# Performance work log

Measured on AMD Instinct MI355X. Metric: run time of the kernel, lower is better.

The kernel has to match this reference:

```python
import jax, jax.numpy as jnp
import numpy as np
from jax import lax


def squash(s):
    # scale = |s|^2/(1+|s|^2); out = scale * s/|s| (eps-stabilized as in source)
    norm = jnp.sum(s * s, axis=-1, keepdims=True)
    return (norm / (1.0 + norm)) * (s / jnp.sqrt(norm + 1e-8))


def setup_inputs() -> dict:
    key = jax.random.key(0)
    k = jax.random.split(key, 4)
    B, H, C = 32, 64, 10
    x = jax.random.normal(k[0], (B, 3, H, H), jnp.float32)
    conv1_w = jax.random.normal(k[1], (256, 3, 9, 9), jnp.float32) * 0.06
    conv1_b = jnp.zeros((256,), jnp.float32)
    conv2_w = jax.random.normal(k[2], (256, 256, 9, 9), jnp.float32) * 0.02  # 256 = 8 caps * 32 routes
    conv2_b = jnp.zeros((256,), jnp.float32)
    route_w = jax.random.normal(k[3], (32, C, 8, 16), jnp.float32)  # [routes, classes, in_dim, out_dim]
    return {"x": x, "conv1_w": conv1_w, "conv1_b": conv1_b,
            "conv2_w": conv2_w, "conv2_b": conv2_b, "route_w": route_w}


def reference(x, conv1_w, conv1_b, conv2_w, conv2_b, route_w):
    dn = ("NCHW", "OIHW", "NCHW")
    # PrimaryCapsules: conv 3->256 k9 s1 + relu
    h = lax.conv_general_dilated(x, conv1_w, (1, 1), "VALID", dimension_numbers=dn)
    h = jax.nn.relu(h + conv1_b[None, :, None, None])
    # CapsuleLayer conv: 256 -> 8*32 k9 s2
    h = lax.conv_general_dilated(h, conv2_w, (2, 2), "VALID", dimension_numbers=dn)
    h = h + conv2_b[None, :, None, None]
    B, _, hh, ww = h.shape
    R, D = 32, 8  # num_routes, capsule dim
    # [B, R*D, h, w] -> [B, R, P, D], squash per capsule vector
    caps = h.reshape(B, R, D, hh, ww).transpose(0, 1, 3, 4, 2).reshape(B, R, hh * ww, D)
    caps = squash(caps)
    # DigitCapsules: per-route linear maps 8->16, shared over spatial positions
    u_hat = jnp.einsum("brpi,rcio->brpco", caps, route_w)  # [B, R, P, C, 16]
    C, O = u_hat.shape[3], u_hat.shape[4]
    u_hat = u_hat.reshape(B, R * hh * ww, C, O)  # [B, N, C, 16]
    b_log = jnp.zeros(u_hat.shape[:-1], u_hat.dtype)  # [B, N, C]
    num_routing = 3
    v = None
    for i in range(num_routing):
        c = jax.nn.softmax(b_log, axis=2)            # over classes (dim=2 in source)
        s = jnp.einsum("bnc,bnco->bco", c, u_hat)    # weighted sum over input caps
        v = squash(s)                                 # [B, C, 16]
        if i < num_routing - 1:
            b_log = b_log + jnp.einsum("bnco,bco->bnc", u_hat, v)  # agreement
    return v
```

## Files before the change

kernel.cpp:

```cpp
#include <hip/hip_runtime.h>
#include <hip/hip_bf16.h>
#include <stdint.h>

typedef __attribute__((ext_vector_type(8))) short short8;
typedef __attribute__((ext_vector_type(4))) float f32x4;
typedef unsigned int u32x4a __attribute__((vector_size(16)));
typedef unsigned int u32x4u __attribute__((vector_size(16), aligned(4)));

__device__ inline unsigned short f2bf(float f) {
    union { float f; uint32_t u; } v; v.f = f;
    uint32_t u = v.u;
    uint32_t r = (u + 0x7FFFu + ((u >> 16) & 1u)) >> 16;
    return (unsigned short)r;
}

__device__ inline void gl_lds16(const unsigned short* g, unsigned short* l) {
    __builtin_amdgcn_global_load_lds(
        (const uint32_t __attribute__((address_space(1)))*)(const void*)g,
        (uint32_t __attribute__((address_space(3)))*)(void*)l, 16, 0, 0);
}

__global__ void cvt_w1(const float* __restrict__ w, unsigned short* __restrict__ A1) {
    int idx = blockIdx.x * 256 + threadIdx.x;
    int row = idx >> 8, k = idx & 255;
    float v = (k < 243) ? w[row * 243 + k] : 0.f;
    A1[idx] = f2bf(v);
}

__global__ void cvt_w2(const float* __restrict__ w, unsigned short* __restrict__ A2t) {
    int idx = blockIdx.x * 256 + threadIdx.x;
    int j = idx & 7;
    int off16 = (idx >> 3) & 1023;
    int tile = idx >> 13;
    int tm = tile / 324, chunk = tile - tm * 324;
    int row = off16 >> 3, sw = off16 & 7;
    int koct = sw ^ (row & 7);
    int kk = chunk * 64 + koct * 8 + j;
    int oc = tm * 128 + row;
    int ic, ky, kx;
    if (kk < 18432) { ic = kk / 72; int rem = kk - ic * 72; ky = rem >> 3; kx = rem & 7; }
    else { int j2 = kk - 18432; ic = j2 / 9; ky = j2 - ic * 9; kx = 8; }
    A2t[idx] = f2bf(w[((oc * 256 + ic) * 9 + ky) * 9 + kx]);
}

__global__ __launch_bounds__(256) void conv1_gemm(
    const unsigned short* __restrict__ A,
    const float* __restrict__ x,
    const float* __restrict__ bias,
    unsigned short* __restrict__ h1)
{
    __shared__ __align__(16) unsigned short As[128 * 40];
    __shared__ __align__(16) unsigned short Bs[128 * 40];
    const int tid = threadIdx.x;
    const int m0 = blockIdx.y * 128;
    const int n0 = blockIdx.x * 128;
    const int lane = tid & 63;
    const int wave = tid >> 6;
    const int wy = wave & 1, wx = wave >> 1;
    const int l16 = lane & 15, q = lane >> 4;

    const int kp = tid & 15;
    const int gn = tid >> 4;
    int baseN[8];
#pragma unroll
    for (int j = 0; j < 8; ++j) {
        int n = n0 + gn * 8 + j;
        int b = n / 3136, p = n % 3136;
        int oy = p / 56, ox = p % 56;
        baseN[j] = b * 12288 + oy * 64 + ox;
    }

    f32x4 acc[4][4];
#pragma unroll
    for (int im = 0; im < 4; ++im)
#pragma unroll
        for (int in = 0; in < 4; ++in)
            acc[im][in] = (f32x4){0.f, 0.f, 0.f, 0.f};

    for (int k0 = 0; k0 < 256; k0 += 32) {
        __syncthreads();
#pragma unroll
        for (int s = 0; s < 2; ++s) {
            int slot = tid + s * 256;
            int row = slot >> 2, seg = slot & 3;
            u32x4a v = *(const u32x4a*)(A + (m0 + row) * 256 + k0 + seg * 8);
            *(u32x4a*)(&As[row * 40 + seg * 8]) = v;
        }
        int ka = k0 + 2 * kp, kb = ka + 1;
        int offa = 0, offb = 0;
        bool va = ka < 243, vb = kb < 243;
        if (va) { int c = ka / 81, t = ka % 81, ky = t / 9, kx = t % 9; offa = c * 4096 + ky * 64 + kx; }
        if (vb) { int c = kb / 81, t = kb % 81, ky = t / 9, kx = t % 9; offb = c * 4096 + ky * 64 + kx; }
#pragma unroll
        for (int j = 0; j < 8; ++j) {
            unsigned int ba = va ? (unsigned int)f2bf(x[baseN[j] + offa]) : 0u;
            unsigned int bb = vb ? (unsigned int)f2bf(x[baseN[j] + offb]) : 0u;
            *(unsigned int*)(&Bs[(gn * 8 + j) * 40 + 2 * kp]) = ba | (bb << 16);
        }
        __syncthreads();

        short8 af[4], bf[4];
#pragma unroll
        for (int im = 0; im < 4; ++im)
            af[im] = *(const short8*)(&As[(wy * 64 + im * 16 + l16) * 40 + q * 8]);
#pragma unroll
        for (int in = 0; in < 4; ++in)
            bf[in] = *(const short8*)(&Bs[(wx * 64 + in * 16 + l16) * 40 + q * 8]);
#pragma unroll
        for (int im = 0; im < 4; ++im)
#pragma unroll
            for (int in = 0; in < 4; ++in)
                acc[im][in] = __builtin_amdgcn_mfma_f32_16x16x32_bf16(af[im], bf[in], acc[im][in], 0, 0, 0);
    }

#pragma unroll
    for (int in = 0; in < 4; ++in) {
        int n = n0 + wx * 64 + in * 16 + l16;
        int b = n / 3136, p = n % 3136;
        int oy = p / 56, ox = p % 56;
#pragma unroll
        for (int im = 0; im < 4; ++im) {
#pragma unroll
            for (int r = 0; r < 4; ++r) {
                int oc = m0 + wy * 64 + im * 16 + q * 4 + r;
                float v = acc[im][in][r] + bias[oc];
                v = v > 0.f ? v : 0.f;
                h1[((b * 256 + oc) * 56 + oy) * 56 + ox] = f2bf(v);
            }
        }
    }
}

#define C2ROW 72
__global__ __launch_bounds__(256) void conv2_gemm(
    const unsigned short* __restrict__ A2t,
    const unsigned short* __restrict__ h1,
    float* __restrict__ c2)
{
    __shared__ __align__(16) unsigned short As[2][8192];
    __shared__ __align__(16) unsigned short Bs[128 * C2ROW];
    const int tid = threadIdx.x;
    const int n0 = blockIdx.x * 128;
    const int z = blockIdx.z;
    const int lane = tid & 63;
    const int wave = tid >> 6;
    const int wy = wave & 1, wx = wave >> 1;
    const int l16 = lane & 15, q = lane >> 4;

    const int oct = tid >> 5;
    int bsrc[4], bdst[4];
#pragma unroll
    for (int i = 0; i < 4; ++i) {
        int n = (tid & 31) + 32 * i;
        int ng = n0 + n;
        int b = ng / 576, p = ng % 576;
        int oy = p / 24, ox = p % 24;
        bsrc[i] = b * 802816 + (2 * oy) * 56 + 2 * ox;
        bdst[i] = n * C2ROW + oct * 8;
    }
    const int tn = tid & 127, thalf = tid >> 7;
    int tbase;
    {
        int ng = n0 + tn;
        int b = ng / 576, p = ng % 576;
        int oy = p / 24, ox = p % 24;
        tbase = b * 802816 + (2 * oy) * 56 + 2 * ox + 8;
    }

    f32x4 acc[4][4];
#pragma unroll
    for (int im = 0; im < 4; ++im)
#pragma unroll
        for (int in = 0; in < 4; ++in)
            acc[im][in] = (f32x4){0.f, 0.f, 0.f, 0.f};

    const size_t tilebase = (size_t)blockIdx.y * 324 * 8192;
    uint32_t bR[16];

    auto issueA = [&](int c, int buf) {
        const unsigned short* at = A2t + tilebase + (size_t)c * 8192;
        int s0 = wave * 4;
#pragma unroll
        for (int i = 0; i < 4; ++i) {
            int sl = (s0 + i) * 64 + lane;
            gl_lds16(at + sl * 8, &As[buf][sl * 8]);
        }
    };
    auto loadB = [&](int c) {
        if (c < 288) {
            int octk = c * 8 + oct;
            int ic = octk / 9, ky = octk - ic * 9;
            int off = ic * 3136 + ky * 56;
#pragma unroll
            for (int i = 0; i < 4; ++i) {
                u32x4u v = *(const u32x4u*)(h1 + bsrc[i] + off);
                bR[4 * i + 0] = v[0]; bR[4 * i + 1] = v[1];
                bR[4 * i + 2] = v[2]; bR[4 * i + 3] = v[3];
            }
        } else {
            int base = c * 64 + thalf * 32 - 18432;
#pragma unroll
            for (int p = 0; p < 16; ++p) {
                int j2 = base + 2 * p;
                int icA = j2 / 9, kyA = j2 - icA * 9;
                int icB = (j2 + 1) / 9, kyB = (j2 + 1) - icB * 9;
                uint32_t ba = h1[tbase + icA * 3136 + kyA * 56];
                uint32_t bb = h1[tbase + icB * 3136 + kyB * 56];
                bR[p] = ba | (bb << 16);
            }
        }
    };
    auto writeB = [&](int c) {
        if (c < 288) {
#pragma unroll
            for (int i = 0; i < 4; ++i) {
                u32x4a v = {bR[4 * i], bR[4 * i + 1], bR[4 * i + 2], bR[4 * i + 3]};
                *(u32x4a*)(&Bs[bdst[i]]) = v;
            }
        } else {
#pragma unroll
            for (int p = 0; p < 16; ++p)
                *(uint32_t*)(&Bs[tn * C2ROW + thalf * 32 + 2 * p]) = bR[p];
        }
    };

    const int nch = (324 - z + 7) >> 3;
    int c = z;
    issueA(c, 0);
    loadB(c);
    for (int i = 0; i < nch; ++i) {
        const int cur = i & 1;
        const int ccur = c, cnext = c + 8;
        __asm__ volatile("s_waitcnt vmcnt(0)" ::: "memory");
        __syncthreads();
        writeB(ccur);
        __syncthreads();
        if (i + 1 < nch) { issueA(cnext, cur ^ 1); loadB(cnext); }
#pragma unroll
        for (int h = 0; h < 2; ++h) {
            short8 af[4], bf[4];
#pragma unroll
            for (int im = 0; im < 4; ++im) {
                int row = wy * 64 + im * 16 + l16;
                int koct = h * 4 + q;
                af[im] = *(const short8*)(&As[cur][(row * 8 + (koct ^ (row & 7))) * 8]);
            }
#pragma unroll
            for (int in = 0; in < 4; ++in)
                bf[in] = *(const short8*)(&Bs[(wx * 64 + in * 16 + l16) * C2ROW + h * 32 + q * 8]);
#pragma unroll
            for (int im = 0; im < 4; ++im)
#pragma unroll
                for (int in = 0; in < 4; ++in)
                    acc[im][in] = __builtin_amdgcn_mfma_f32_16x16x32_bf16(af[im], bf[in], acc[im][in], 0, 0, 0);
        }
        c = cnext;
    }

    const int m0 = blockIdx.y * 128;
#pragma unroll
    for (int in = 0; in < 4; ++in) {
        int nn = n0 + wx * 64 + in * 16 + l16;
        int bb = nn / 576, pp = nn % 576;
#pragma unroll
        for (int im = 0; im < 4; ++im) {
#pragma unroll
            for (int r = 0; r < 4; ++r) {
                int oc = m0 + wy * 64 + im * 16 + q * 4 + r;
                atomicAdd(&c2[(bb * 256 + oc) * 576 + pp], acc[im][in][r]);
            }
        }
    }
}

__global__ void squash_caps(const float* __restrict__ c2, const float* __restrict__ bias,
                            float* __restrict__ caps) {
    int idx = blockIdx.x * 256 + threadIdx.x;
    int b = idx / 18432;
    int rp = idx % 18432;
    int r = rp / 576, p = rp % 576;
    float s[8]; float n2 = 0.f;
#pragma unroll
    for (int d = 0; d < 8; ++d) {
        s[d] = c2[(b * 256 + r * 8 + d) * 576 + p] + bias[r * 8 + d];
        n2 += s[d] * s[d];
    }
    float sc = (n2 / (1.f + n2)) / sqrtf(n2 + 1e-8f);
#pragma unroll
    for (int d = 0; d < 8; ++d)
        caps[idx * 8 + d] = sc * s[d];
}

__global__ __launch_bounds__(64) void capsum0(const float* __restrict__ caps,
                                              float* __restrict__ G) {
    int r = blockIdx.x, b = blockIdx.y;
    const float* cp = caps + (size_t)(b * 32 + r) * 4608;
    int tid = threadIdx.x;
    f32x4 s0 = (f32x4){0.f, 0.f, 0.f, 0.f}, s1 = s0;
    for (int jv = 0; jv < 9; ++jv) {
        const f32x4* qp = (const f32x4*)(cp + (jv * 64 + tid) * 8);
        s0 += qp[0]; s1 += qp[1];
    }
#pragma unroll
    for (int off = 32; off > 0; off >>= 1) {
#pragma unroll
        for (int k = 0; k < 4; ++k) {
            s0[k] += __shfl_down(s0[k], off, 64);
            s1[k] += __shfl_down(s1[k], off, 64);
        }
    }
    if (tid == 0) {
        float g[8] = {s0[0], s0[1], s0[2], s0[3], s1[0], s1[1], s1[2], s1[3]};
        float* gp = G + (size_t)((b * 32 + r) * 10) * 8;
        for (int cc = 0; cc < 10; ++cc)
#pragma unroll
            for (int ii = 0; ii < 8; ++ii) gp[cc * 8 + ii] = g[ii] * 0.1f;
    }
}

__global__ __launch_bounds__(64) void route_accum(const float* __restrict__ caps,
                                                  const float* __restrict__ W,
                                                  const float* __restrict__ V,
                                                  float* __restrict__ G) {
    int r = blockIdx.x, b = blockIdx.y;
    __shared__ float wv[80];
    __shared__ float red[80][64];
    int tid = threadIdx.x;
    for (int v = tid; v < 80; v += 64) {
        int cc = v >> 3, ii = v & 7;
        float s = 0.f;
#pragma unroll
        for (int o = 0; o < 16; ++o)
            s += W[((r * 10 + cc) * 8 + ii) * 16 + o] * V[(b * 10 + cc) * 16 + o];
        wv[v] = s;
    }
    __syncthreads();
    float g[80];
#pragma unroll
    for (int v = 0; v < 80; ++v) g[v] = 0.f;
    const float* cp = caps + (size_t)(b * 32 + r) * 4608;
    for (int j = 0; j < 9; ++j) {
        int p = j * 64 + tid;
        const f32x4* qp = (const f32x4*)(cp + p * 8);
        f32x4 c0 = qp[0], c1 = qp[1];
        float c8[8];
#pragma unroll
        for (int i = 0; i < 4; ++i) { c8[i] = c0[i]; c8[4 + i] = c1[i]; }
        float a[10]; float m = -1e30f;
#pragma unroll
        for (int cc = 0; cc < 10; ++cc) {
            float t = 0.f;
#pragma unroll
            for (int i = 0; i < 8; ++i) t += c8[i] * wv[cc * 8 + i];
            a[cc] = t; m = fmaxf(m, t);
        }
        float sum = 0.f;
#pragma unroll
        for (int cc = 0; cc < 10; ++cc) { a[cc] = __expf(a[cc] - m); sum += a[cc]; }
        float inv = 1.f / sum;
#pragma unroll
        for (int cc = 0; cc < 10; ++cc) {
            float w = a[cc] * inv;
#pragma unroll
            for (int i = 0; i < 8; ++i) g[cc * 8 + i] += w * c8[i];
        }
    }
#pragma unroll
    for (int v = 0; v < 80; ++v) red[v][tid] = g[v];
    __syncthreads();
    for (int v = tid; v < 80; v += 64) {
        float s = 0.f;
        for (int t = 0; t < 64; ++t) s += red[v][t];
        G[(b * 32 + r) * 80 + v] = s;
    }
}

__global__ __launch_bounds__(160) void sv_kernel(const float* __restrict__ G,
                                                 const float* __restrict__ W,
                                                 float* __restrict__ V,
                                                 float* __restrict__ out, int last) {
    int b = blockIdx.x;
    int c = threadIdx.x / 16, o = threadIdx.x % 16;
    __shared__ float sL[10][16];
    float s = 0.f;
    for (int r = 0; r < 32; ++r) {
        const float* g = G + ((b * 32 + r) * 10 + c) * 8;
        const float* w = W + ((r * 10 + c) * 8) * 16 + o;
#pragma unroll
        for (int i = 0; i < 8; ++i) s += g[i] * w[i * 16];
    }
    sL[c][o] = s;
    __syncthreads();
    float n2 = 0.f;
#pragma unroll
    for (int oo = 0; oo < 16; ++oo) { float t = sL[c][oo]; n2 += t * t; }
    float sc = (n2 / (1.f + n2)) / sqrtf(n2 + 1e-8f);
    float v = sc * s;
    V[(b * 10 + c) * 16 + o] += v;
    if (last) out[(b * 10 + c) * 16 + o] = v;
}

extern "C" void kernel_launch(void* const* d_in, const int* in_sizes, int n_in,
                              void* d_out, int out_size, void* d_ws, size_t ws_size,
                              hipStream_t stream) {
    const float* x  = (const float*)d_in[0];
    const float* w1 = (const float*)d_in[1];
    const float* b1 = (const float*)d_in[2];
    const float* w2 = (const float*)d_in[3];
    const float* b2 = (const float*)d_in[4];
    const float* rw = (const float*)d_in[5];

    char* ws = (char*)d_ws;
    unsigned short* A1   = (unsigned short*)(ws);
    unsigned short* A2   = (unsigned short*)(ws + 262144);
    unsigned short* h1   = (unsigned short*)(ws + 10878976);
    float*          c2   = (float*)(ws + 62259200);
    float*          caps = (float*)(ws + 81133568);
    float*          V    = (float*)(ws + 100007936);
    float*          G    = (float*)(ws + 100028416);

    hipLaunchKernelGGL(cvt_w1, dim3(256), dim3(256), 0, stream, w1, A1);
    hipLaunchKernelGGL(cvt_w2, dim3(20736), dim3(256), 0, stream, w2, A2);
    hipMemsetAsync(c2, 0, 18874368, stream);
    hipLaunchKernelGGL(conv1_gemm, dim3(784, 2), dim3(256), 0, stream, A1, x, b1, h1);
    hipLaunchKernelGGL(conv2_gemm, dim3(144, 2, 8), dim3(256), 0, stream, A2, h1, c2);
    hipLaunchKernelGGL(squash_caps, dim3(2304), dim3(256), 0, stream, c2, b2, caps);
    hipMemsetAsync(V, 0, 5120 * sizeof(float), stream);
    hipLaunchKernelGGL(capsum0, dim3(32, 32), dim3(64), 0, stream, caps, G);
    hipLaunchKernelGGL(sv_kernel, dim3(32), dim3(160), 0, stream, G, rw, V, (float*)d_out, 0);
    for (int it = 1; it < 3; ++it) {
        hipLaunchKernelGGL(route_accum, dim3(32, 32), dim3(64), 0, stream, caps, rw, V, G);
        hipLaunchKernelGGL(sv_kernel, dim3(32), dim3(160), 0, stream, G, rw, V,
                           (float*)d_out, it == 2 ? 1 : 0);
    }
}
```

Before: 471.8 us.

## Load conv2 MFMA fragments directly from global memory, dropping LDS staging

Conv2's GEMM no longer stages A and B tiles through shared memory. Weights are pre-laid-out in MFMA fragment order so each lane loads its A fragment directly, and B fragments are gathered straight from h1 into registers. A two-stage register double buffer overlaps the next chunk's loads with the current MFMAs, and occupancy is hinted at 2 blocks per CU. This removes LDS writes, barriers and syncs, but each wave now fetches its own fragments with no sharing across waves, which raises global/L2 traffic and register pressure.

```diff
diff --git a/kernel.cpp b/kernel.cpp
--- a/kernel.cpp
+++ b/kernel.cpp
@@ -14,12 +14,6 @@
     return (unsigned short)r;
 }
 
-__device__ inline void gl_lds16(const unsigned short* g, unsigned short* l) {
-    __builtin_amdgcn_global_load_lds(
-        (const uint32_t __attribute__((address_space(1)))*)(const void*)g,
-        (uint32_t __attribute__((address_space(3)))*)(void*)l, 16, 0, 0);
-}
-
 __global__ void cvt_w1(const float* __restrict__ w, unsigned short* __restrict__ A1) {
     int idx = blockIdx.x * 256 + threadIdx.x;
     int row = idx >> 8, k = idx & 255;
@@ -27,20 +21,21 @@
     A1[idx] = f2bf(v);
 }
 
-__global__ void cvt_w2(const float* __restrict__ w, unsigned short* __restrict__ A2t) {
+__global__ void cvt_w2(const float* __restrict__ w, unsigned short* __restrict__ A2f) {
     int idx = blockIdx.x * 256 + threadIdx.x;
     int j = idx & 7;
-    int off16 = (idx >> 3) & 1023;
-    int tile = idx >> 13;
-    int tm = tile / 324, chunk = tile - tm * 324;
-    int row = off16 >> 3, sw = off16 & 7;
-    int koct = sw ^ (row & 7);
-    int kk = chunk * 64 + koct * 8 + j;
-    int oc = tm * 128 + row;
+    int lane = (idx >> 3) & 63;
+    int im = (idx >> 9) & 3;
+    int h = (idx >> 11) & 1;
+    int gc = idx >> 12;
+    int g = gc / 324, c = gc - g * 324;
+    int l16 = lane & 15, q = lane >> 4;
+    int row = g * 64 + im * 16 + l16;
+    int kk = c * 64 + (h * 4 + q) * 8 + j;
     int ic, ky, kx;
     if (kk < 18432) { ic = kk / 72; int rem = kk - ic * 72; ky = rem >> 3; kx = rem & 7; }
     else { int j2 = kk - 18432; ic = j2 / 9; ky = j2 - ic * 9; kx = 8; }
-    A2t[idx] = f2bf(w[((oc * 256 + ic) * 9 + ky) * 9 + kx]);
+    A2f[idx] = f2bf(w[((row * 256 + ic) * 9 + ky) * 9 + kx]);
 }
 
 __global__ __launch_bounds__(256) void conv1_gemm(
@@ -131,41 +126,29 @@
     }
 }
 
-#define C2ROW 72
-__global__ __launch_bounds__(256) void conv2_gemm(
-    const unsigned short* __restrict__ A2t,
+__global__ __launch_bounds__(256, 2) void conv2_gemm(
+    const unsigned short* __restrict__ A2f,
     const unsigned short* __restrict__ h1,
     float* __restrict__ c2)
 {
-    __shared__ __align__(16) unsigned short As[2][8192];
-    __shared__ __align__(16) unsigned short Bs[128 * C2ROW];
     const int tid = threadIdx.x;
     const int n0 = blockIdx.x * 128;
+    const int y = blockIdx.y;
     const int z = blockIdx.z;
     const int lane = tid & 63;
     const int wave = tid >> 6;
     const int wy = wave & 1, wx = wave >> 1;
     const int l16 = lane & 15, q = lane >> 4;
 
-    const int oct = tid >> 5;
-    int bsrc[4], bdst[4];
-#pragma unroll
-    for (int i = 0; i < 4; ++i) {
-        int n = (tid & 31) + 32 * i;
-        int ng = n0 + n;
-        int b = ng / 576, p = ng % 576;
+    const unsigned short* bptr[4];
+#pragma unroll
+    for (int in = 0; in < 4; ++in) {
+        int n = n0 + wx * 64 + in * 16 + l16;
+        int b = n / 576, p = n % 576;
         int oy = p / 24, ox = p % 24;
-        bsrc[i] = b * 802816 + (2 * oy) * 56 + 2 * ox;
-        bdst[i] = n * C2ROW + oct * 8;
-    }
-    const int tn = tid & 127, thalf = tid >> 7;
-    int tbase;
-    {
-        int ng = n0 + tn;
-        int b = ng / 576, p = ng % 576;
-        int oy = p / 24, ox = p % 24;
-        tbase = b * 802816 + (2 * oy) * 56 + 2 * ox + 8;
-    }
+        bptr[in] = h1 + b * 802816 + (2 * oy) * 56 + 2 * ox;
+    }
+    const unsigned short* abase = A2f + (size_t)(y * 2 + wy) * 324 * 4096 + lane * 8;
 
     f32x4 acc[4][4];
 #pragma unroll
@@ -174,90 +157,78 @@
         for (int in = 0; in < 4; ++in)
             acc[im][in] = (f32x4){0.f, 0.f, 0.f, 0.f};
 
-    const size_t tilebase = (size_t)blockIdx.y * 324 * 8192;
-    uint32_t bR[16];
-
-    auto issueA = [&](int c, int buf) {
-        const unsigned short* at = A2t + tilebase + (size_t)c * 8192;
-        int s0 = wave * 4;
-#pragma unroll
-        for (int i = 0; i < 4; ++i) {
-            int sl = (s0 + i) * 64 + lane;
-            gl_lds16(at + sl * 8, &As[buf][sl * 8]);
-        }
+    auto loadA = [&](int c, short8 (&af)[2][4]) {
+        const unsigned short* ab = abase + (size_t)c * 4096;
+#pragma unroll
+        for (int h = 0; h < 2; ++h)
+#pragma unroll
+            for (int im = 0; im < 4; ++im)
+                af[h][im] = *(const short8*)(ab + (h * 4 + im) * 512);
     };
-    auto loadB = [&](int c) {
-        if (c < 288) {
-            int octk = c * 8 + oct;
-            int ic = octk / 9, ky = octk - ic * 9;
+    auto loadBmain = [&](int c, short8 (&bf)[2][4]) {
+#pragma unroll
+        for (int h = 0; h < 2; ++h) {
+            int octk = c * 8 + h * 4 + q;
+            int ic = octk / 9;
+            int ky = octk - ic * 9;
             int off = ic * 3136 + ky * 56;
 #pragma unroll
-            for (int i = 0; i < 4; ++i) {
-                u32x4u v = *(const u32x4u*)(h1 + bsrc[i] + off);
-                bR[4 * i + 0] = v[0]; bR[4 * i + 1] = v[1];
-                bR[4 * i + 2] = v[2]; bR[4 * i + 3] = v[3];
+            for (int in = 0; in < 4; ++in) {
+                u32x4u v = *(const u32x4u*)(bptr[in] + off);
+                bf[h][in] = __builtin_bit_cast(short8, v);
             }
-        } else {
-            int base = c * 64 + thalf * 32 - 18432;
-#pragma unroll
-            for (int p = 0; p < 16; ++p) {
-                int j2 = base + 2 * p;
-                int icA = j2 / 9, kyA = j2 - icA * 9;
-                int icB = (j2 + 1) / 9, kyB = (j2 + 1) - icB * 9;
-                uint32_t ba = h1[tbase + icA * 3136 + kyA * 56];
-                uint32_t bb = h1[tbase + icB * 3136 + kyB * 56];
-                bR[p] = ba | (bb << 16);
+        }
+    };
+    auto loadBtail = [&](int c, short8 (&bf)[2][4]) {
+#pragma unroll
+        for (int h = 0; h < 2; ++h) {
+            int j2o = c * 64 + (h * 4 + q) * 8 - 18432;
+            int offs[8];
+#pragma unroll
+            for (int j = 0; j < 8; ++j) {
+                int j2 = j2o + j;
+                int ic = j2 / 9, ky = j2 - ic * 9;
+                offs[j] = 8 + ic * 3136 + ky * 56;
             }
+#pragma unroll
+            for (int in = 0; in < 4; ++in) {
+                short8 v;
+#pragma unroll
+                for (int j = 0; j < 8; ++j) v[j] = (short)bptr[in][offs[j]];
+                bf[h][in] = v;
+            }
         }
     };
-    auto writeB = [&](int c) {
-        if (c < 288) {
-#pragma unroll
-            for (int i = 0; i < 4; ++i) {
-                u32x4a v = {bR[4 * i], bR[4 * i + 1], bR[4 * i + 2], bR[4 * i + 3]};
-                *(u32x4a*)(&Bs[bdst[i]]) = v;
-            }
-        } else {
-#pragma unroll
-            for (int p = 0; p < 16; ++p)
-                *(uint32_t*)(&Bs[tn * C2ROW + thalf * 32 + 2 * p]) = bR[p];
-        }
+    auto loadAB = [&](int c, short8 (&af)[2][4], short8 (&bf)[2][4]) {
+        loadA(c, af);
+        if (c < 288) loadBmain(c, bf); else loadBtail(c, bf);
     };
+    auto computeC = [&](short8 (&af)[2][4], short8 (&bf)[2][4]) {
+#pragma unroll
+        for (int h = 0; h < 2; ++h)
+#pragma unroll
+            for (int im = 0; im < 4; ++im)
+#pragma unroll
+                for (int in = 0; in < 4; ++in)
+                    acc[im][in] = __builtin_amdgcn_mfma_f32_16x16x32_bf16(
+                        af[h][im], bf[h][in], acc[im][in], 0, 0, 0);
+    };
 
     const int nch = (324 - z + 7) >> 3;
-    int c = z;
-    issueA(c, 0);
-    loadB(c);
-    for (int i = 0; i < nch; ++i) {
-        const int cur = i & 1;
-        const int ccur = c, cnext = c + 8;
-        __asm__ volatile("s_waitcnt vmcnt(0)" ::: "memory");
-        __syncthreads();
-        writeB(ccur);
-        __syncthreads();
-        if (i + 1 < nch) { issueA(cnext, cur ^ 1); loadB(cnext); }
-#pragma unroll
-        for (int h = 0; h < 2; ++h) {
-            short8 af[4], bf[4];
-#pragma unroll
-            for (int im = 0; im < 4; ++im) {
-                int row = wy * 64 + im * 16 + l16;
-                int koct = h * 4 + q;
-                af[im] = *(const short8*)(&As[cur][(row * 8 + (koct ^ (row & 7))) * 8]);
-            }
-#pragma unroll
-            for (int in = 0; in < 4; ++in)
-                bf[in] = *(const short8*)(&Bs[(wx * 64 + in * 16 + l16) * C2ROW + h * 32 + q * 8]);
-#pragma unroll
-            for (int im = 0; im < 4; ++im)
-#pragma unroll
-                for (int in = 0; in < 4; ++in)
-                    acc[im][in] = __builtin_amdgcn_mfma_f32_16x16x32_bf16(af[im], bf[in], acc[im][in], 0, 0, 0);
-        }
-        c = cnext;
-    }
-
-    const int m0 = blockIdx.y * 128;
+    short8 a0[2][4], b0[2][4], a1[2][4], b1[2][4];
+    int i = 0, c = z;
+    loadAB(c, a0, b0);
+    while (true) {
+        if (i + 1 < nch) loadAB(c + 8, a1, b1);
+        computeC(a0, b0);
+        if (i + 1 >= nch) break;
+        if (i + 2 < nch) loadAB(c + 16, a0, b0);
+        computeC(a1, b1);
+        if (i + 2 >= nch) break;
+        i += 2; c += 16;
+    }
+
+    const int m0 = y * 128;
 #pragma unroll
     for (int in = 0; in < 4; ++in) {
         int nn = n0 + wx * 64 + in * 16 + l16;
```

New measurement: 1.001 ms. 112% more time.

## Load conv2 B fragments straight to registers and double-buffer with split barriers

Applied to the files above, without the earlier changes.

In the main K loop, conv2_gemm now loads im2col B fragments from global memory directly into per-lane MFMA registers, no longer staging them through LDS. Two register sets and two A LDS buffers are ping-ponged, with partial vmcnt waits and raw s_barrier in place of full syncs. MFMA blocks are wrapped in s_setprio. The aim is to drop the LDS round trip and one __syncthreads per chunk and to overlap loads with compute. The tail chunks keep the old LDS path, and the register use is higher.

```diff
diff --git a/kernel.cpp b/kernel.cpp
--- a/kernel.cpp
+++ b/kernel.cpp
@@ -131,14 +131,13 @@
     }
 }
 
-#define C2ROW 72
 __global__ __launch_bounds__(256) void conv2_gemm(
     const unsigned short* __restrict__ A2t,
     const unsigned short* __restrict__ h1,
     float* __restrict__ c2)
 {
     __shared__ __align__(16) unsigned short As[2][8192];
-    __shared__ __align__(16) unsigned short Bs[128 * C2ROW];
+    __shared__ __align__(16) unsigned short BsT[128 * 72];
     const int tid = threadIdx.x;
     const int n0 = blockIdx.x * 128;
     const int z = blockIdx.z;
@@ -147,16 +146,13 @@
     const int wy = wave & 1, wx = wave >> 1;
     const int l16 = lane & 15, q = lane >> 4;
 
-    const int oct = tid >> 5;
-    int bsrc[4], bdst[4];
-#pragma unroll
-    for (int i = 0; i < 4; ++i) {
-        int n = (tid & 31) + 32 * i;
-        int ng = n0 + n;
-        int b = ng / 576, p = ng % 576;
+    int boff[4];
+#pragma unroll
+    for (int in = 0; in < 4; ++in) {
+        int n = n0 + wx * 64 + in * 16 + l16;
+        int b = n / 576, p = n % 576;
         int oy = p / 24, ox = p % 24;
-        bsrc[i] = b * 802816 + (2 * oy) * 56 + 2 * ox;
-        bdst[i] = n * C2ROW + oct * 8;
+        boff[in] = b * 802816 + (2 * oy) * 56 + 2 * ox;
     }
     const int tn = tid & 127, thalf = tid >> 7;
     int tbase;
@@ -175,7 +171,6 @@
             acc[im][in] = (f32x4){0.f, 0.f, 0.f, 0.f};
 
     const size_t tilebase = (size_t)blockIdx.y * 324 * 8192;
-    uint32_t bR[16];
 
     auto issueA = [&](int c, int buf) {
         const unsigned short* at = A2t + tilebase + (size_t)c * 8192;
@@ -186,75 +181,113 @@
             gl_lds16(at + sl * 8, &As[buf][sl * 8]);
         }
     };
-    auto loadB = [&](int c) {
-        if (c < 288) {
-            int octk = c * 8 + oct;
-            int ic = octk / 9, ky = octk - ic * 9;
+    auto loadBmain = [&](int c, short8 (&B)[2][4]) {
+#pragma unroll
+        for (int h = 0; h < 2; ++h) {
+            int octk = c * 8 + h * 4 + q;
+            int ic = octk / 9;
+            int ky = octk - ic * 9;
             int off = ic * 3136 + ky * 56;
 #pragma unroll
-            for (int i = 0; i < 4; ++i) {
-                u32x4u v = *(const u32x4u*)(h1 + bsrc[i] + off);
-                bR[4 * i + 0] = v[0]; bR[4 * i + 1] = v[1];
-                bR[4 * i + 2] = v[2]; bR[4 * i + 3] = v[3];
+            for (int in = 0; in < 4; ++in) {
+                u32x4u v = *(const u32x4u*)(h1 + boff[in] + off);
+                B[h][in] = __builtin_bit_cast(short8, v);
             }
-        } else {
-            int base = c * 64 + thalf * 32 - 18432;
-#pragma unroll
-            for (int p = 0; p < 16; ++p) {
-                int j2 = base + 2 * p;
-                int icA = j2 / 9, kyA = j2 - icA * 9;
-                int icB = (j2 + 1) / 9, kyB = (j2 + 1) - icB * 9;
-                uint32_t ba = h1[tbase + icA * 3136 + kyA * 56];
-                uint32_t bb = h1[tbase + icB * 3136 + kyB * 56];
-                bR[p] = ba | (bb << 16);
-            }
         }
     };
-    auto writeB = [&](int c) {
-        if (c < 288) {
-#pragma unroll
-            for (int i = 0; i < 4; ++i) {
-                u32x4a v = {bR[4 * i], bR[4 * i + 1], bR[4 * i + 2], bR[4 * i + 3]};
-                *(u32x4a*)(&Bs[bdst[i]]) = v;
-            }
-        } else {
-#pragma unroll
-            for (int p = 0; p < 16; ++p)
-                *(uint32_t*)(&Bs[tn * C2ROW + thalf * 32 + 2 * p]) = bR[p];
-        }
-    };
-
-    const int nch = (324 - z + 7) >> 3;
-    int c = z;
-    issueA(c, 0);
-    loadB(c);
-    for (int i = 0; i < nch; ++i) {
-        const int cur = i & 1;
-        const int ccur = c, cnext = c + 8;
-        __asm__ volatile("s_waitcnt vmcnt(0)" ::: "memory");
-        __syncthreads();
-        writeB(ccur);
-        __syncthreads();
-        if (i + 1 < nch) { issueA(cnext, cur ^ 1); loadB(cnext); }
+    auto computeChunk = [&](int buf, short8 (&B)[2][4]) {
 #pragma unroll
         for (int h = 0; h < 2; ++h) {
-            short8 af[4], bf[4];
+            short8 af[4];
 #pragma unroll
             for (int im = 0; im < 4; ++im) {
                 int row = wy * 64 + im * 16 + l16;
                 int koct = h * 4 + q;
-                af[im] = *(const short8*)(&As[cur][(row * 8 + (koct ^ (row & 7))) * 8]);
+                af[im] = *(const short8*)(&As[buf][(row * 8 + (koct ^ (row & 7))) * 8]);
             }
+            __builtin_amdgcn_s_setprio(1);
+#pragma unroll
+            for (int im = 0; im < 4; ++im)
+#pragma unroll
+                for (int in = 0; in < 4; ++in)
+                    acc[im][in] = __builtin_amdgcn_mfma_f32_16x16x32_bf16(
+                        af[h == 0 ? im : im], B[h][in], acc[im][in], 0, 0, 0);
+            __builtin_amdgcn_s_setprio(0);
+        }
+    };
+
+    short8 B0[2][4], B1[2][4];
+
+    issueA(z, 0);
+    loadBmain(z, B0);
+    __asm__ volatile("s_waitcnt vmcnt(8)" ::: "memory");
+    __builtin_amdgcn_s_barrier();
+    __asm__ volatile("" ::: "memory");
+
+    int c = z;
+    for (int it = 0; it < 18; ++it) {
+        issueA(c + 8, 1);
+        loadBmain(c + 8, B1);
+        __asm__ volatile("" ::: "memory");
+        computeChunk(0, B0);
+        __asm__ volatile("s_waitcnt vmcnt(8)" ::: "memory");
+        __builtin_amdgcn_s_barrier();
+        __asm__ volatile("" ::: "memory");
+
+        if (it < 17) {
+            issueA(c + 16, 0);
+            loadBmain(c + 16, B0);
+        } else {
+            issueA(z + 288, 0);
+        }
+        __asm__ volatile("" ::: "memory");
+        computeChunk(1, B1);
+        __asm__ volatile("s_waitcnt vmcnt(8)" ::: "memory");
+        __builtin_amdgcn_s_barrier();
+        __asm__ volatile("" ::: "memory");
+        c += 16;
+    }
+
+    int bt = 0;
+    for (int ct = z + 288; ct < 324; ct += 8) {
+        uint32_t bR[16];
+        int base = ct * 64 + thalf * 32 - 18432;
+#pragma unroll
+        for (int p = 0; p < 16; ++p) {
+            int j2 = base + 2 * p;
+            int icA = j2 / 9, kyA = j2 - icA * 9;
+            int icB = (j2 + 1) / 9, kyB = (j2 + 1) - icB * 9;
+            uint32_t ba = h1[tbase + icA * 3136 + kyA * 56];
+            uint32_t bb = h1[tbase + icB * 3136 + kyB * 56];
+            bR[p] = ba | (bb << 16);
+        }
+        if (ct + 8 < 324) issueA(ct + 8, bt ^ 1);
+        __syncthreads();
+#pragma unroll
+        for (int p = 0; p < 16; ++p)
+            *(uint32_t*)(&BsT[tn * 72 + thalf * 32 + 2 * p]) = bR[p];
+        __syncthreads();
+#pragma unroll
+        for (int h = 0; h < 2; ++h) {
+            short8 af[4], bf[4];
+#pragma unroll
+            for (int im = 0; im < 4; ++im) {
+                int row = wy * 64 + im * 16 + l16;
+                int koct = h * 4 + q;
+                af[im] = *(const short8*)(&As[bt][(row * 8 + (koct ^ (row & 7))) * 8]);
+            }
 #pragma unroll
             for (int in = 0; in < 4; ++in)
-                bf[in] = *(const short8*)(&Bs[(wx * 64 + in * 16 + l16) * C2ROW + h * 32 + q * 8]);
+                bf[in] = *(const short8*)(&BsT[(wx * 64 + in * 16 + l16) * 72 + h * 32 + q * 8]);
 #pragma unroll
             for (int im = 0; im < 4; ++im)
 #pragma unroll
                 for (int in = 0; in < 4; ++in)
-                    acc[im][in] = __builtin_amdgcn_mfma_f32_16x16x32_bf16(af[im], bf[in], acc[im][in], 0, 0, 0);
-        }
-        c = cnext;
+                    acc[im][in] = __builtin_amdgcn_mfma_f32_16x16x32_bf16(
+                        af[im], bf[in], acc[im][in], 0, 0, 0);
+        }
+        __syncthreads();
+        bt ^= 1;
     }
 
     const int m0 = blockIdx.y * 128;
```

After: 511.2 us. 1.08x slower.

## Enlarge conv2 GEMM tile to 256x256 with 512 threads and contiguous split-K

Applied to the files above, without the earlier changes.

The conv2 implicit GEMM now uses 512-thread blocks computing a 256x256 output tile (all output channels) with a swizzled LDS layout for both A and B, double-buffered in 128KB of dynamic shared memory. Split-K is restructured into 18 contiguous 18-chunk ranges per block, with the ragged tail handled in a separate branch, and the weight repacking is changed to match. Block indices are remapped in both conv kernels for better cache locality, and s_setprio is placed around the MFMA groups. The aim is to raise arithmetic intensity and cut redundant B loads and atomics. In exchange it uses heavier register and LDS pressure, which allows at most two blocks per CU.

```diff
diff --git a/kernel.cpp b/kernel.cpp
--- a/kernel.cpp
+++ b/kernel.cpp
@@ -27,20 +27,18 @@
     A1[idx] = f2bf(v);
 }
 
-__global__ void cvt_w2(const float* __restrict__ w, unsigned short* __restrict__ A2t) {
+__global__ void cvt_w2(const float* __restrict__ w, unsigned short* __restrict__ A2c) {
     int idx = blockIdx.x * 256 + threadIdx.x;
     int j = idx & 7;
-    int off16 = (idx >> 3) & 1023;
-    int tile = idx >> 13;
-    int tm = tile / 324, chunk = tile - tm * 324;
-    int row = off16 >> 3, sw = off16 & 7;
+    int sw = (idx >> 3) & 7;
+    int row = (idx >> 6) & 255;
+    int chunk = idx >> 14;
     int koct = sw ^ (row & 7);
     int kk = chunk * 64 + koct * 8 + j;
-    int oc = tm * 128 + row;
     int ic, ky, kx;
     if (kk < 18432) { ic = kk / 72; int rem = kk - ic * 72; ky = rem >> 3; kx = rem & 7; }
     else { int j2 = kk - 18432; ic = j2 / 9; ky = j2 - ic * 9; kx = 8; }
-    A2t[idx] = f2bf(w[((oc * 256 + ic) * 9 + ky) * 9 + kx]);
+    A2c[idx] = f2bf(w[((row * 256 + ic) * 9 + ky) * 9 + kx]);
 }
 
 __global__ __launch_bounds__(256) void conv1_gemm(
@@ -53,7 +51,8 @@
     __shared__ __align__(16) unsigned short Bs[128 * 40];
     const int tid = threadIdx.x;
     const int m0 = blockIdx.y * 128;
-    const int n0 = blockIdx.x * 128;
+    const int sx = (blockIdx.x & 7) * 98 + (blockIdx.x >> 3);
+    const int n0 = sx * 128;
     const int lane = tid & 63;
     const int wave = tid >> 6;
     const int wy = wave & 1, wx = wave >> 1;
@@ -131,142 +130,184 @@
     }
 }
 
-#define C2ROW 72
-__global__ __launch_bounds__(256) void conv2_gemm(
-    const unsigned short* __restrict__ A2t,
+__global__ __launch_bounds__(512, 2) void conv2_gemm(
+    const unsigned short* __restrict__ A2c,
     const unsigned short* __restrict__ h1,
     float* __restrict__ c2)
 {
-    __shared__ __align__(16) unsigned short As[2][8192];
-    __shared__ __align__(16) unsigned short Bs[128 * C2ROW];
+    extern __shared__ __align__(16) unsigned short lds[];
+    unsigned short* AsB = lds;
+    unsigned short* BsB = lds + 32768;
     const int tid = threadIdx.x;
-    const int n0 = blockIdx.x * 128;
+    const int sx = (blockIdx.x & 7) * 9 + (blockIdx.x >> 3);
+    const int n0 = sx * 256;
     const int z = blockIdx.z;
     const int lane = tid & 63;
     const int wave = tid >> 6;
-    const int wy = wave & 1, wx = wave >> 1;
+    const int wy = wave >> 2;
+    const int wx = wave & 3;
     const int l16 = lane & 15, q = lane >> 4;
 
-    const int oct = tid >> 5;
-    int bsrc[4], bdst[4];
+    int aoffA[8][2];
+#pragma unroll
+    for (int im = 0; im < 8; ++im)
+#pragma unroll
+        for (int h = 0; h < 2; ++h) {
+            int row = wy * 128 + im * 16 + l16;
+            aoffA[im][h] = (row * 8 + ((h * 4 + q) ^ (row & 7))) * 8;
+        }
+    int boffL[4][2];
+#pragma unroll
+    for (int in = 0; in < 4; ++in)
+#pragma unroll
+        for (int h = 0; h < 2; ++h) {
+            int n = wx * 64 + in * 16 + l16;
+            boffL[in][h] = (n * 8 + ((h * 4 + q) ^ (n & 7))) * 8;
+        }
+
+    const int sn = lane >> 3;
+    const int koctS = (lane & 7) ^ sn;
+    int bsrc[4];
 #pragma unroll
     for (int i = 0; i < 4; ++i) {
-        int n = (tid & 31) + 32 * i;
+        int n = (wave * 4 + i) * 8 + sn;
         int ng = n0 + n;
         int b = ng / 576, p = ng % 576;
         int oy = p / 24, ox = p % 24;
         bsrc[i] = b * 802816 + (2 * oy) * 56 + 2 * ox;
-        bdst[i] = n * C2ROW + oct * 8;
-    }
-    const int tn = tid & 127, thalf = tid >> 7;
-    int tbase;
-    {
-        int ng = n0 + tn;
-        int b = ng / 576, p = ng % 576;
-        int oy = p / 24, ox = p % 24;
-        tbase = b * 802816 + (2 * oy) * 56 + 2 * ox + 8;
-    }
-
-    f32x4 acc[4][4];
-#pragma unroll
-    for (int im = 0; im < 4; ++im)
+    }
+
+    f32x4 acc[8][4];
+#pragma unroll
+    for (int im = 0; im < 8; ++im)
 #pragma unroll
         for (int in = 0; in < 4; ++in)
             acc[im][in] = (f32x4){0.f, 0.f, 0.f, 0.f};
 
-    const size_t tilebase = (size_t)blockIdx.y * 324 * 8192;
-    uint32_t bR[16];
-
-    auto issueA = [&](int c, int buf) {
-        const unsigned short* at = A2t + tilebase + (size_t)c * 8192;
-        int s0 = wave * 4;
+    auto issueA = [&](int c, unsigned short* dst) {
+        const unsigned short* at = A2c + (size_t)c * 16384;
 #pragma unroll
         for (int i = 0; i < 4; ++i) {
-            int sl = (s0 + i) * 64 + lane;
-            gl_lds16(at + sl * 8, &As[buf][sl * 8]);
+            int sl = (wave * 4 + i) * 64 + lane;
+            gl_lds16(at + sl * 8, dst + sl * 8);
         }
     };
-    auto loadB = [&](int c) {
-        if (c < 288) {
-            int octk = c * 8 + oct;
-            int ic = octk / 9, ky = octk - ic * 9;
-            int off = ic * 3136 + ky * 56;
-#pragma unroll
-            for (int i = 0; i < 4; ++i) {
-                u32x4u v = *(const u32x4u*)(h1 + bsrc[i] + off);
-                bR[4 * i + 0] = v[0]; bR[4 * i + 1] = v[1];
-                bR[4 * i + 2] = v[2]; bR[4 * i + 3] = v[3];
+    auto bloadMain = [&](int c, short8 (&R)[4]) {
+        int octk = c * 8 + koctS;
+        int ic = octk / 9, ky = octk - 9 * ic;
+        int koff = ic * 3136 + ky * 56;
+#pragma unroll
+        for (int i = 0; i < 4; ++i) {
+            u32x4u v = *(const u32x4u*)(h1 + bsrc[i] + koff);
+            R[i] = __builtin_bit_cast(short8, v);
+        }
+    };
+    auto bwriteMain = [&](short8 (&R)[4], unsigned short* dst) {
+#pragma unroll
+        for (int i = 0; i < 4; ++i) {
+            int sl = (wave * 4 + i) * 64 + lane;
+            *(short8*)(dst + sl * 8) = R[i];
+        }
+    };
+    auto computeChunk = [&](const unsigned short* Ab, const unsigned short* Bb) {
+        short8 bf[4][2];
+#pragma unroll
+        for (int in = 0; in < 4; ++in)
+#pragma unroll
+            for (int h = 0; h < 2; ++h)
+                bf[in][h] = *(const short8*)(Bb + boffL[in][h]);
+#pragma unroll
+        for (int im = 0; im < 8; ++im) {
+            short8 a0 = *(const short8*)(Ab + aoffA[im][0]);
+            short8 a1 = *(const short8*)(Ab + aoffA[im][1]);
+            __builtin_amdgcn_s_setprio(1);
+#pragma unroll
+            for (int in = 0; in < 4; ++in) {
+                acc[im][in] = __builtin_amdgcn_mfma_f32_16x16x32_bf16(a0, bf[in][0], acc[im][in], 0, 0, 0);
+                acc[im][in] = __builtin_amdgcn_mfma_f32_16x16x32_bf16(a1, bf[in][1], acc[im][in], 0, 0, 0);
             }
-        } else {
-            int base = c * 64 + thalf * 32 - 18432;
-#pragma unroll
-            for (int p = 0; p < 16; ++p) {
-                int j2 = base + 2 * p;
-                int icA = j2 / 9, kyA = j2 - icA * 9;
-                int icB = (j2 + 1) / 9, kyB = (j2 + 1) - icB * 9;
-                uint32_t ba = h1[tbase + icA * 3136 + kyA * 56];
-                uint32_t bb = h1[tbase + icB * 3136 + kyB * 56];
-                bR[p] = ba | (bb << 16);
+            __builtin_amdgcn_s_setprio(0);
+        }
+    };
+
+    short8 R[4];
+
+    if (z < 16) {
+        const int c0 = z * 18;
+        bloadMain(c0, R);
+        issueA(c0, AsB);
+        bwriteMain(R, BsB);
+        __syncthreads();
+        for (int t = 0; t < 18; ++t) {
+            const int p = t & 1;
+            unsigned short* Ap = AsB + p * 16384;
+            unsigned short* Bp = BsB + p * 16384;
+            unsigned short* An = AsB + (p ^ 1) * 16384;
+            unsigned short* Bn = BsB + (p ^ 1) * 16384;
+            if (t < 17) { bloadMain(c0 + t + 1, R); issueA(c0 + t + 1, An); }
+            computeChunk(Ap, Bp);
+            if (t < 17) bwriteMain(R, Bn);
+            __syncthreads();
+        }
+    } else {
+        const int c0 = 288 + (z - 16) * 18;
+        int tb[4], kbase[4];
+#pragma unroll
+        for (int k = 0; k < 4; ++k) {
+            int s = tid * 4 + k;
+            int n = s >> 3, sw = s & 7;
+            int koct = sw ^ (n & 7);
+            int ng = n0 + n;
+            int b = ng / 576, pp = ng % 576;
+            int oy = pp / 24, ox = pp % 24;
+            tb[k] = b * 802816 + (2 * oy) * 56 + 2 * ox + 8;
+            kbase[k] = koct * 8;
+        }
+        auto bloadTail = [&](int c, short8 (&T)[4]) {
+#pragma unroll
+            for (int k = 0; k < 4; ++k) {
+                int ob = c * 64 + kbase[k] - 18432;
+                short8 v;
+#pragma unroll
+                for (int j = 0; j < 8; ++j) {
+                    int j2 = ob + j;
+                    int ic = j2 / 9, ky = j2 - 9 * ic;
+                    v[j] = (short)h1[tb[k] + ic * 3136 + ky * 56];
+                }
+                T[k] = v;
             }
-        }
-    };
-    auto writeB = [&](int c) {
-        if (c < 288) {
-#pragma unroll
-            for (int i = 0; i < 4; ++i) {
-                u32x4a v = {bR[4 * i], bR[4 * i + 1], bR[4 * i + 2], bR[4 * i + 3]};
-                *(u32x4a*)(&Bs[bdst[i]]) = v;
-            }
-        } else {
-#pragma unroll
-            for (int p = 0; p < 16; ++p)
-                *(uint32_t*)(&Bs[tn * C2ROW + thalf * 32 + 2 * p]) = bR[p];
-        }
-    };
-
-    const int nch = (324 - z + 7) >> 3;
-    int c = z;
-    issueA(c, 0);
-    loadB(c);
-    for (int i = 0; i < nch; ++i) {
-        const int cur = i & 1;
-        const int ccur = c, cnext = c + 8;
-        __asm__ volatile("s_waitcnt vmcnt(0)" ::: "memory");
+        };
+        auto bwriteTail = [&](short8 (&T)[4], unsigned short* dst) {
+#pragma unroll
+            for (int k = 0; k < 4; ++k)
+                *(short8*)(dst + (tid * 4 + k) * 8) = T[k];
+        };
+        bloadTail(c0, R);
+        issueA(c0, AsB);
+        bwriteTail(R, BsB);
         __syncthreads();
-        writeB(ccur);
-        __syncthreads();
-        if (i + 1 < nch) { issueA(cnext, cur ^ 1); loadB(cnext); }
-#pragma unroll
-        for (int h = 0; h < 2; ++h) {
-            short8 af[4], bf[4];
-#pragma unroll
-            for (int im = 0; im < 4; ++im) {
-                int row = wy * 64 + im * 16 + l16;
-                int koct = h * 4 + q;
-                af[im] = *(const short8*)(&As[cur][(row * 8 + (koct ^ (row & 7))) * 8]);
-            }
-#pragma unroll
-            for (int in = 0; in < 4; ++in)
-                bf[in] = *(const short8*)(&Bs[(wx * 64 + in * 16 + l16) * C2ROW + h * 32 + q * 8]);
-#pragma unroll
-            for (int im = 0; im < 4; ++im)
-#pragma unroll
-                for (int in = 0; in < 4; ++in)
-                    acc[im][in] = __builtin_amdgcn_mfma_f32_16x16x32_bf16(af[im], bf[in], acc[im][in], 0, 0, 0);
-        }
-        c = cnext;
-    }
-
-    const int m0 = blockIdx.y * 128;
+        for (int t = 0; t < 18; ++t) {
+            const int p = t & 1;
+            unsigned short* Ap = AsB + p * 16384;
+            unsigned short* Bp = BsB + p * 16384;
+            unsigned short* An = AsB + (p ^ 1) * 16384;
+            unsigned short* Bn = BsB + (p ^ 1) * 16384;
+            if (t < 17) { bloadTail(c0 + t + 1, R); issueA(c0 + t + 1, An); }
+            computeChunk(Ap, Bp);
+            if (t < 17) bwriteTail(R, Bn);
+            __syncthreads();
+        }
+    }
+
 #pragma unroll
     for (int in = 0; in < 4; ++in) {
         int nn = n0 + wx * 64 + in * 16 + l16;
         int bb = nn / 576, pp = nn % 576;
 #pragma unroll
-        for (int im = 0; im < 4; ++im) {
+        for (int im = 0; im < 8; ++im) {
 #pragma unroll
             for (int r = 0; r < 4; ++r) {
-                int oc = m0 + wy * 64 + im * 16 + q * 4 + r;
+                int oc = wy * 128 + im * 16 + q * 4 + r;
                 atomicAdd(&c2[(bb * 256 + oc) * 576 + pp], acc[im][in][r]);
             }
         }
@@ -419,11 +460,14 @@
     float*          V    = (float*)(ws + 100007936);
     float*          G    = (float*)(ws + 100028416);
 
+    hipFuncSetAttribute((const void*)conv2_gemm,
+                        hipFuncAttributeMaxDynamicSharedMemorySize, 131072);
+
     hipLaunchKernelGGL(cvt_w1, dim3(256), dim3(256), 0, stream, w1, A1);
     hipLaunchKernelGGL(cvt_w2, dim3(20736), dim3(256), 0, stream, w2, A2);
     hipMemsetAsync(c2, 0, 18874368, stream);
     hipLaunchKernelGGL(conv1_gemm, dim3(784, 2), dim3(256), 0, stream, A1, x, b1, h1);
-    hipLaunchKernelGGL(conv2_gemm, dim3(144, 2, 8), dim3(256), 0, stream, A2, h1, c2);
+    hipLaunchKernelGGL(conv2_gemm, dim3(72, 1, 18), dim3(512), 131072, stream, A2, h1, c2);
     hipLaunchKernelGGL(squash_caps, dim3(2304), dim3(256), 0, stream, c2, b2, caps);
     hipMemsetAsync(V, 0, 5120 * sizeof(float), stream);
     hipLaunchKernelGGL(capsum0, dim3(32, 32), dim3(64), 0, stream, caps, G);
```

New measurement: 671.8 us. 42.4% more time.
